# Performance work log

Hardware: AMD Instinct MI355X
Metric: run time of the kernel (lower is better)

Reference implementation:

```python
import jax, jax.numpy as jnp
import numpy as np

DIM = 256
WIN = 8          # window height == width
HEADS = 8
HEAD_DIM = DIM // HEADS
NW = 64          # number of windows per image
B_IMG = 16
N = WIN * WIN    # 64 tokens per window
B_ = B_IMG * NW  # 1024


def _relative_position_index():
    # matches torch.meshgrid default (ij) indexing
    coords = np.stack(np.meshgrid(np.arange(WIN), np.arange(WIN), indexing='ij'))  # [2,Wh,Ww]
    flat = coords.reshape(2, -1)                                # [2,N]
    rel = flat[:, :, None] - flat[:, None, :]                   # [2,N,N]
    rel = rel.transpose(1, 2, 0).copy()                         # [N,N,2]
    rel[:, :, 0] += WIN - 1
    rel[:, :, 1] += WIN - 1
    rel[:, :, 0] *= 2 * WIN - 1
    return rel.sum(-1).astype(np.int32)                         # [N,N]


def setup_inputs() -> dict:
    key = jax.random.key(0)
    ks = jax.random.split(key, 24)
    std = 0.02

    def lin(i):
        W = jax.random.normal(ks[i], (DIM, DIM), jnp.float32) * std
        b = jax.random.normal(ks[i + 1], (DIM,), jnp.float32) * std
        return W, b

    Wq, bq = lin(0)
    Wk, bk = lin(2)
    Wv, bv = lin(4)
    Wvs, bvs = lin(6)      # v_scale
    Wvh, bvh = lin(8)      # v_shift
    Wpx, bpx = lin(10)     # proj_x
    Wps, bps = lin(12)     # proj_scale
    Wph, bph = lin(14)     # proj_shift

    bias_table = jax.random.normal(ks[16], ((2 * WIN - 1) * (2 * WIN - 1), HEADS), jnp.float32) * std
    rel_idx = jnp.asarray(_relative_position_index())

    q_input = jax.random.normal(ks[17], (B_, N, DIM), jnp.float32)
    k_input = jax.random.normal(ks[18], (B_, N, DIM), jnp.float32)
    v_input = jax.random.normal(ks[19], (B_, N, DIM), jnp.float32)
    scale_in = jax.random.normal(ks[20], (B_, N, DIM), jnp.float32)
    shift_in = jax.random.normal(ks[21], (B_, N, DIM), jnp.float32)

    # shifted-window style mask: 0 where attendable, large negative otherwise
    u = jax.random.uniform(ks[22], (NW, N, N), jnp.float32)
    mask = jnp.where(u < 0.15, -100.0, 0.0).astype(jnp.float32)

    return {
        'q_input': q_input, 'k_input': k_input, 'v_input': v_input,
        'scale_in': scale_in, 'shift_in': shift_in, 'mask': mask,
        'Wq': Wq, 'bq': bq, 'Wk': Wk, 'bk': bk, 'Wv': Wv, 'bv': bv,
        'Wvs': Wvs, 'bvs': bvs, 'Wvh': Wvh, 'bvh': bvh,
        'Wpx': Wpx, 'bpx': bpx, 'Wps': Wps, 'bps': bps, 'Wph': Wph, 'bph': bph,
        'bias_table': bias_table, 'rel_idx': rel_idx,
    }


def reference(q_input, k_input, v_input, scale_in, shift_in, mask,
              Wq, bq, Wk, bk, Wv, bv, Wvs, bvs, Wvh, bvh,
              Wpx, bpx, Wps, bps, Wph, bph, bias_table, rel_idx):
    B, Ntok, C = q_input.shape
    scale = HEAD_DIM ** -0.5

    def to_heads(x, W, b):
        # nn.Linear: x @ W.T + b, then split heads -> [B, H, N, hd]
        return (x @ W.T + b).reshape(B, Ntok, HEADS, HEAD_DIM).transpose(0, 2, 1, 3)

    q = to_heads(q_input, Wq, bq) * scale
    k = to_heads(k_input, Wk, bk)
    v = to_heads(v_input, Wv, bv)
    v_scale = to_heads(scale_in, Wvs, bvs)
    v_shift = to_heads(shift_in, Wvh, bvh)

    attn = jnp.einsum('bhnd,bhmd->bhnm', q, k)                    # [B,H,N,N]
    rel_bias = bias_table[rel_idx]                                # [N,N,H] gather
    attn = attn + rel_bias.transpose(2, 0, 1)[None]               # add per-head bias

    nW = mask.shape[0]
    attn = attn.reshape(B // nW, nW, HEADS, Ntok, Ntok) + mask[None, :, None]
    attn = jax.nn.softmax(attn.reshape(B, HEADS, Ntok, Ntok), axis=-1)

    def out_proj(val, Wp, bp):
        o = jnp.einsum('bhnm,bhmd->bhnd', attn, val)
        o = o.transpose(0, 2, 1, 3).reshape(B, Ntok, C)
        return o @ Wp.T + bp

    x_out = out_proj(v, Wpx, bpx)
    scale_out = out_proj(v_scale, Wps, bps)
    shift_out = out_proj(v_shift, Wph, bph)
    return (x_out, scale_out, shift_out)
```

## Files before the change

kernel.cpp:

```cpp
#include <hip/hip_runtime.h>


typedef __attribute__((ext_vector_type(8))) __bf16 bf16x8;
typedef __attribute__((ext_vector_type(4))) float f32x4;
typedef __attribute__((ext_vector_type(4))) unsigned short u16x4;

#define LOFF_QS 16384
#define LOFF_KS 32768
#define LOFF_PS 49152

__device__ __forceinline__ unsigned short f2bf(float f) {
  unsigned int u = __float_as_uint(f);
  u += 0x7FFFu + ((u >> 16) & 1u);
  return (unsigned short)(u >> 16);
}

__device__ __forceinline__ int swz256(int row, int col) {
  return row * 256 + (col ^ ((row & 31) << 3));
}
__device__ __forceinline__ int swz64(int row, int col) {
  return row * 64 + (col ^ ((row & 7) << 3));
}

__global__ void pack_weights(const float* __restrict__ W0, const float* __restrict__ W1,
                             const float* __restrict__ W2, const float* __restrict__ W3,
                             const float* __restrict__ W4, const float* __restrict__ W5,
                             const float* __restrict__ W6, const float* __restrict__ W7,
                             unsigned short* __restrict__ pk) {
  int t = blockIdx.x * 256 + threadIdx.x;
  int wsel = t >> 13;
  int rem  = t & 8191;
  int cb   = rem >> 9;
  int kc   = (rem >> 6) & 7;
  int l    = rem & 63;
  const float* W = (wsel == 0) ? W0 : (wsel == 1) ? W1 : (wsel == 2) ? W2 : (wsel == 3) ? W3
                 : (wsel == 4) ? W4 : (wsel == 5) ? W5 : (wsel == 6) ? W6 : W7;
  int row = cb * 16 + (l & 15);
  int col = kc * 32 + ((l >> 4) << 3);
  const float* src = W + row * 256 + col;
  unsigned short* dst = pk + (size_t)t * 8;
#pragma unroll
  for (int i = 0; i < 8; ++i) dst[i] = f2bf(src[i]);
}

__global__ void make_bm(const float* __restrict__ mask, const float* __restrict__ btab,
                        const int* __restrict__ ridx, float* __restrict__ bm) {
  int t = blockIdx.x * 256 + threadIdx.x;
  int j = t & 63;
  int i = (t >> 6) & 63;
  int h = (t >> 12) & 7;
  int wi = t >> 15;
  bm[t] = mask[(wi * 64 + i) * 64 + j] + btab[ridx[i * 64 + j] * 8 + h];
}

__device__ __forceinline__ void stage_x(unsigned short* XS, const float* __restrict__ X,
                                        int b, int tid) {
  const float4* src = reinterpret_cast<const float4*>(X + (size_t)b * 16384);
#pragma unroll
  for (int it = 0; it < 8; ++it) {
    int f = it * 512 + tid;
    float4 v = src[f];
    int row = f >> 6;
    int col = (f & 63) << 2;
    u16x4 p;
    p[0] = f2bf(v.x); p[1] = f2bf(v.y); p[2] = f2bf(v.z); p[3] = f2bf(v.w);
    *reinterpret_cast<u16x4*>(XS + swz256(row, col)) = p;
  }
}

__device__ __forceinline__ void proj_core(const unsigned short* __restrict__ aTile,
                                          const unsigned short* __restrict__ pw,
                                          const float* __restrict__ bias, float scale,
                                          int lane, int w, f32x4 acc[4][2]) {
  const int r16 = lane & 15, c4 = lane >> 4;
  f32x4 z = {0.f, 0.f, 0.f, 0.f};
#pragma unroll
  for (int mf = 0; mf < 4; ++mf)
#pragma unroll
    for (int nf = 0; nf < 2; ++nf) acc[mf][nf] = z;
#pragma unroll
  for (int kc = 0; kc < 8; ++kc) {
    bf16x8 a[4];
#pragma unroll
    for (int mf = 0; mf < 4; ++mf) {
      int row = mf * 16 + r16;
      int col = kc * 32 + (c4 << 3);
      a[mf] = *reinterpret_cast<const bf16x8*>(aTile + swz256(row, col));
    }
    bf16x8 bb[2];
#pragma unroll
    for (int nf = 0; nf < 2; ++nf)
      bb[nf] = *reinterpret_cast<const bf16x8*>(pw + ((((2 * w + nf) * 8 + kc) * 64 + lane) << 3));
#pragma unroll
    for (int mf = 0; mf < 4; ++mf)
#pragma unroll
      for (int nf = 0; nf < 2; ++nf)
        acc[mf][nf] = __builtin_amdgcn_mfma_f32_16x16x32_bf16(a[mf], bb[nf], acc[mf][nf], 0, 0, 0);
  }
  float b0 = bias[w * 32 + r16];
  float b1 = bias[w * 32 + 16 + r16];
#pragma unroll
  for (int mf = 0; mf < 4; ++mf)
#pragma unroll
    for (int r = 0; r < 4; ++r) {
      acc[mf][0][r] = (acc[mf][0][r] + b0) * scale;
      acc[mf][1][r] = (acc[mf][1][r] + b1) * scale;
    }
}

__device__ __forceinline__ void store_rm_bf16(unsigned short* dst, const f32x4 acc[4][2],
                                              int lane, int w) {
  const int r16 = lane & 15, c4 = lane >> 4;
#pragma unroll
  for (int mf = 0; mf < 4; ++mf)
#pragma unroll
    for (int nf = 0; nf < 2; ++nf)
#pragma unroll
      for (int r = 0; r < 4; ++r) {
        int row = mf * 16 + c4 * 4 + r;
        int col = w * 32 + nf * 16 + r16;
        dst[swz256(row, col)] = f2bf(acc[mf][nf][r]);
      }
}

__device__ __forceinline__ void store_tr_bf16(unsigned short* dst, const f32x4 acc[4][2],
                                              int lane, int w) {
  const int r16 = lane & 15, c4 = lane >> 4;
#pragma unroll
  for (int mf = 0; mf < 4; ++mf)
#pragma unroll
    for (int nf = 0; nf < 2; ++nf)
#pragma unroll
      for (int r = 0; r < 4; ++r) {
        int vrow = w * 32 + nf * 16 + r16;
        int vcol = mf * 16 + c4 * 4 + r;
        dst[swz64(vrow, vcol)] = f2bf(acc[mf][nf][r]);
      }
}

__device__ __forceinline__ void store_gl_f32(float* __restrict__ dst, const f32x4 acc[4][2],
                                             int lane, int w) {
  const int r16 = lane & 15, c4 = lane >> 4;
#pragma unroll
  for (int mf = 0; mf < 4; ++mf)
#pragma unroll
    for (int nf = 0; nf < 2; ++nf)
#pragma unroll
      for (int r = 0; r < 4; ++r) {
        int row = mf * 16 + c4 * 4 + r;
        int col = w * 32 + nf * 16 + r16;
        dst[row * 256 + col] = acc[mf][nf][r];
      }
}

__device__ __forceinline__ void attn_core(const unsigned short* __restrict__ sm,
                                          const float* __restrict__ bmw,
                                          int lane, int w, unsigned short* Ps) {
  const int r16 = lane & 15, c4 = lane >> 4;
  const unsigned short* Qs = sm + LOFF_QS;
  const unsigned short* Ks = sm + LOFF_KS;
  bf16x8 aq[4], bk4[4];
#pragma unroll
  for (int mf = 0; mf < 4; ++mf)
    aq[mf] = *reinterpret_cast<const bf16x8*>(Qs + swz256(mf * 16 + r16, w * 32 + (c4 << 3)));
#pragma unroll
  for (int nf = 0; nf < 4; ++nf)
    bk4[nf] = *reinterpret_cast<const bf16x8*>(Ks + swz256(nf * 16 + r16, w * 32 + (c4 << 3)));
  f32x4 z = {0.f, 0.f, 0.f, 0.f};
  f32x4 s[4][4];
#pragma unroll
  for (int mf = 0; mf < 4; ++mf)
#pragma unroll
    for (int nf = 0; nf < 4; ++nf)
      s[mf][nf] = __builtin_amdgcn_mfma_f32_16x16x32_bf16(aq[mf], bk4[nf], z, 0, 0, 0);
#pragma unroll
  for (int mf = 0; mf < 4; ++mf)
#pragma unroll
    for (int r = 0; r < 4; ++r) {
      int row = mf * 16 + c4 * 4 + r;
      const float* bp = bmw + row * 64 + r16;
      float v0 = s[mf][0][r] + bp[0];
      float v1 = s[mf][1][r] + bp[16];
      float v2 = s[mf][2][r] + bp[32];
      float v3 = s[mf][3][r] + bp[48];
      float m = fmaxf(fmaxf(v0, v1), fmaxf(v2, v3));
      m = fmaxf(m, __shfl_xor(m, 1));
      m = fmaxf(m, __shfl_xor(m, 2));
      m = fmaxf(m, __shfl_xor(m, 4));
      m = fmaxf(m, __shfl_xor(m, 8));
      float e0 = __expf(v0 - m), e1 = __expf(v1 - m);
      float e2 = __expf(v2 - m), e3 = __expf(v3 - m);
      float sum = e0 + e1 + e2 + e3;
      sum += __shfl_xor(sum, 1);
      sum += __shfl_xor(sum, 2);
      sum += __shfl_xor(sum, 4);
      sum += __shfl_xor(sum, 8);
      float inv = 1.0f / sum;
      Ps[swz64(row, r16)]      = f2bf(e0 * inv);
      Ps[swz64(row, r16 + 16)] = f2bf(e1 * inv);
      Ps[swz64(row, r16 + 32)] = f2bf(e2 * inv);
      Ps[swz64(row, r16 + 48)] = f2bf(e3 * inv);
    }
}

__device__ __forceinline__ void pv_core(const unsigned short* __restrict__ Ps,
                                        const unsigned short* __restrict__ Vt,
                                        int lane, int w, f32x4 o[4][2]) {
  const int r16 = lane & 15, c4 = lane >> 4;
  f32x4 z = {0.f, 0.f, 0.f, 0.f};
#pragma unroll
  for (int mf = 0; mf < 4; ++mf)
#pragma unroll
    for (int nf = 0; nf < 2; ++nf) o[mf][nf] = z;
#pragma unroll
  for (int kc = 0; kc < 2; ++kc) {
    bf16x8 a[4];
#pragma unroll
    for (int mf = 0; mf < 4; ++mf)
      a[mf] = *reinterpret_cast<const bf16x8*>(Ps + swz64(mf * 16 + r16, kc * 32 + (c4 << 3)));
    bf16x8 bb[2];
#pragma unroll
    for (int nf = 0; nf < 2; ++nf)
      bb[nf] = *reinterpret_cast<const bf16x8*>(Vt + swz64(w * 32 + nf * 16 + r16, kc * 32 + (c4 << 3)));
#pragma unroll
    for (int mf = 0; mf < 4; ++mf)
#pragma unroll
      for (int nf = 0; nf < 2; ++nf)
        o[mf][nf] = __builtin_amdgcn_mfma_f32_16x16x32_bf16(a[mf], bb[nf], o[mf][nf], 0, 0, 0);
  }
}

__global__ __launch_bounds__(512, 2) void win_attn(
    const float* __restrict__ gq, const float* __restrict__ gk, const float* __restrict__ gv,
    const float* __restrict__ gsc, const float* __restrict__ gsh,
    const unsigned short* __restrict__ pk,
    const float* __restrict__ b_q, const float* __restrict__ b_k, const float* __restrict__ b_v,
    const float* __restrict__ b_vs, const float* __restrict__ b_vh,
    const float* __restrict__ b_px, const float* __restrict__ b_ps, const float* __restrict__ b_ph,
    const float* __restrict__ bm, float* __restrict__ out) {
  __shared__ __align__(16) unsigned short sm[81920];
  const int b    = blockIdx.x;
  const int tid  = threadIdx.x;
  const int lane = tid & 63;
  const int w    = tid >> 6;

  unsigned short* XS = sm;
  unsigned short* QS = sm + LOFF_QS;
  unsigned short* KS = sm + LOFF_KS;
  unsigned short* PS = sm + LOFF_PS + w * 4096;

  f32x4 acc[4][2];

  stage_x(XS, gq, b, tid);
  __syncthreads();
  proj_core(XS, pk, b_q, 0.17677669529663687f, lane, w, acc);
  store_rm_bf16(QS, acc, lane, w);
  __syncthreads();
  stage_x(XS, gk, b, tid);
  __syncthreads();
  proj_core(XS, pk + 65536, b_k, 1.0f, lane, w, acc);
  store_rm_bf16(KS, acc, lane, w);
  __syncthreads();
  stage_x(XS, gv, b, tid);
  attn_core(sm, bm + (size_t)(((b & 63) * 8 + w) << 12), lane, w, PS);
  __syncthreads();
  proj_core(XS, pk + 2 * 65536, b_v, 1.0f, lane, w, acc);
  store_tr_bf16(QS, acc, lane, w);
  __syncthreads();
  stage_x(XS, gsc, b, tid);
  {
    f32x4 o[4][2];
    pv_core(PS, QS, lane, w, o);
    store_rm_bf16(KS, o, lane, w);
  }
  __syncthreads();
  proj_core(KS, pk + 5 * 65536, b_px, 1.0f, lane, w, acc);
  store_gl_f32(out + (size_t)b * 16384, acc, lane, w);
  proj_core(XS, pk + 3 * 65536, b_vs, 1.0f, lane, w, acc);
  store_tr_bf16(QS, acc, lane, w);
  __syncthreads();
  stage_x(XS, gsh, b, tid);
  {
    f32x4 o[4][2];
    pv_core(PS, QS, lane, w, o);
    store_rm_bf16(KS, o, lane, w);
  }
  __syncthreads();
  proj_core(KS, pk + 6 * 65536, b_ps, 1.0f, lane, w, acc);
  store_gl_f32(out + 16777216 + (size_t)b * 16384, acc, lane, w);
  proj_core(XS, pk + 4 * 65536, b_vh, 1.0f, lane, w, acc);
  store_tr_bf16(QS, acc, lane, w);
  __syncthreads();
  {
    f32x4 o[4][2];
    pv_core(PS, QS, lane, w, o);
    store_rm_bf16(KS, o, lane, w);
  }
  __syncthreads();
  proj_core(KS, pk + 7 * 65536, b_ph, 1.0f, lane, w, acc);
  store_gl_f32(out + 33554432 + (size_t)b * 16384, acc, lane, w);
}

extern "C" void kernel_launch(void* const* d_in, const int* in_sizes, int n_in,
                              void* d_out, int out_size, void* d_ws, size_t ws_size,
                              hipStream_t stream) {
  const float* Xq   = (const float*)d_in[0];
  const float* Xk   = (const float*)d_in[1];
  const float* Xv   = (const float*)d_in[2];
  const float* Xsc  = (const float*)d_in[3];
  const float* Xsh  = (const float*)d_in[4];
  const float* mask = (const float*)d_in[5];
  const float* Wq   = (const float*)d_in[6];  const float* bq  = (const float*)d_in[7];
  const float* Wk   = (const float*)d_in[8];  const float* bk  = (const float*)d_in[9];
  const float* Wv   = (const float*)d_in[10]; const float* bv  = (const float*)d_in[11];
  const float* Wvs  = (const float*)d_in[12]; const float* bvs = (const float*)d_in[13];
  const float* Wvh  = (const float*)d_in[14]; const float* bvh = (const float*)d_in[15];
  const float* Wpx  = (const float*)d_in[16]; const float* bpx = (const float*)d_in[17];
  const float* Wps  = (const float*)d_in[18]; const float* bps = (const float*)d_in[19];
  const float* Wph  = (const float*)d_in[20]; const float* bph = (const float*)d_in[21];
  const float* btab = (const float*)d_in[22];
  const int*   ridx = (const int*)d_in[23];

  unsigned short* pk = (unsigned short*)d_ws;
  float* bm = (float*)((char*)d_ws + (size_t)8 * 65536 * 2);

  pack_weights<<<256, 256, 0, stream>>>(Wq, Wk, Wv, Wvs, Wvh, Wpx, Wps, Wph, pk);
  make_bm<<<8192, 256, 0, stream>>>(mask, btab, ridx, bm);
  win_attn<<<1024, 512, 0, stream>>>(Xq, Xk, Xv, Xsc, Xsh, pk,
                                     bq, bk, bv, bvs, bvh, bpx, bps, bph,
                                     bm, (float*)d_out);
}
```

Baseline: 215.3 us.

## Prefetch input tiles into registers to overlap global loads with MFMA compute

Global loads of each input tile are split from the bf16 conversion and LDS write. Loads are issued into register double buffers (rA/rB) one or two stages ahead, so HBM latency is hidden behind projection MFMAs and several barriers disappear. The K tile is staged into the P buffer region before attention runs. The bias+mask table is also re-laid out so each lane reads one float4 instead of four scalars, and bf16 conversion now uses the native cast. This costs 64 extra VGPRs per thread for the two buffers, which may cause spills or lower occupancy under launch_bounds(512,2).

Result: slower. 226.3 us (+5.1%).

```diff
diff --git a/kernel.cpp b/kernel.cpp
--- a/kernel.cpp
+++ b/kernel.cpp
@@ -2,6 +2,7 @@
 
 
 typedef __attribute__((ext_vector_type(8))) __bf16 bf16x8;
+typedef __attribute__((ext_vector_type(4))) __bf16 bf16x4;
 typedef __attribute__((ext_vector_type(4))) float f32x4;
 typedef __attribute__((ext_vector_type(4))) unsigned short u16x4;
 
@@ -10,9 +11,12 @@
 #define LOFF_PS 49152
 
 __device__ __forceinline__ unsigned short f2bf(float f) {
-  unsigned int u = __float_as_uint(f);
-  u += 0x7FFFu + ((u >> 16) & 1u);
-  return (unsigned short)(u >> 16);
+  return __builtin_bit_cast(unsigned short, (__bf16)f);
+}
+__device__ __forceinline__ u16x4 cvt4(float4 v) {
+  bf16x4 h;
+  h[0] = (__bf16)v.x; h[1] = (__bf16)v.y; h[2] = (__bf16)v.z; h[3] = (__bf16)v.w;
+  return __builtin_bit_cast(u16x4, h);
 }
 
 __device__ __forceinline__ int swz256(int row, int col) {
@@ -50,21 +54,24 @@
   int i = (t >> 6) & 63;
   int h = (t >> 12) & 7;
   int wi = t >> 15;
-  bm[t] = mask[(wi * 64 + i) * 64 + j] + btab[ridx[i * 64 + j] * 8 + h];
-}
-
-__device__ __forceinline__ void stage_x(unsigned short* XS, const float* __restrict__ X,
-                                        int b, int tid) {
+  float v = mask[(wi * 64 + i) * 64 + j] + btab[ridx[i * 64 + j] * 8 + h];
+  int idx = (((wi * 8 + h) * 64 + i) * 16 + (j & 15)) * 4 + (j >> 4);
+  bm[idx] = v;
+}
+
+__device__ __forceinline__ void load_tile(float4 r[8], const float* __restrict__ X,
+                                          int b, int tid) {
   const float4* src = reinterpret_cast<const float4*>(X + (size_t)b * 16384);
+#pragma unroll
+  for (int it = 0; it < 8; ++it) r[it] = src[it * 512 + tid];
+}
+__device__ __forceinline__ void write_tile(unsigned short* XS, const float4 r[8], int tid) {
 #pragma unroll
   for (int it = 0; it < 8; ++it) {
     int f = it * 512 + tid;
-    float4 v = src[f];
     int row = f >> 6;
     int col = (f & 63) << 2;
-    u16x4 p;
-    p[0] = f2bf(v.x); p[1] = f2bf(v.y); p[2] = f2bf(v.z); p[3] = f2bf(v.w);
-    *reinterpret_cast<u16x4*>(XS + swz256(row, col)) = p;
+    *reinterpret_cast<u16x4*>(XS + swz256(row, col)) = cvt4(r[it]);
   }
 }
 
@@ -178,11 +185,11 @@
 #pragma unroll
     for (int r = 0; r < 4; ++r) {
       int row = mf * 16 + c4 * 4 + r;
-      const float* bp = bmw + row * 64 + r16;
-      float v0 = s[mf][0][r] + bp[0];
-      float v1 = s[mf][1][r] + bp[16];
-      float v2 = s[mf][2][r] + bp[32];
-      float v3 = s[mf][3][r] + bp[48];
+      float4 bp4 = *reinterpret_cast<const float4*>(bmw + row * 64 + (r16 << 2));
+      float v0 = s[mf][0][r] + bp4.x;
+      float v1 = s[mf][1][r] + bp4.y;
+      float v2 = s[mf][2][r] + bp4.z;
+      float v3 = s[mf][3][r] + bp4.w;
       float m = fmaxf(fmaxf(v0, v1), fmaxf(v2, v3));
       m = fmaxf(m, __shfl_xor(m, 1));
       m = fmaxf(m, __shfl_xor(m, 2));
@@ -247,44 +254,50 @@
   unsigned short* XS = sm;
   unsigned short* QS = sm + LOFF_QS;
   unsigned short* KS = sm + LOFF_KS;
+  unsigned short* PB = sm + LOFF_PS;
   unsigned short* PS = sm + LOFF_PS + w * 4096;
 
   f32x4 acc[4][2];
-
-  stage_x(XS, gq, b, tid);
-  __syncthreads();
+  float4 rA[8], rB[8];
+
+  load_tile(rA, gq, b, tid);
+  load_tile(rB, gk, b, tid);
+  write_tile(XS, rA, tid);
+  __syncthreads();
+  load_tile(rA, gv, b, tid);
   proj_core(XS, pk, b_q, 0.17677669529663687f, lane, w, acc);
   store_rm_bf16(QS, acc, lane, w);
-  __syncthreads();
-  stage_x(XS, gk, b, tid);
-  __syncthreads();
-  proj_core(XS, pk + 65536, b_k, 1.0f, lane, w, acc);
+  write_tile(PB, rB, tid);
+  __syncthreads();
+  load_tile(rB, gsc, b, tid);
+  proj_core(PB, pk + 65536, b_k, 1.0f, lane, w, acc);
   store_rm_bf16(KS, acc, lane, w);
-  __syncthreads();
-  stage_x(XS, gv, b, tid);
+  write_tile(XS, rA, tid);
+  __syncthreads();
   attn_core(sm, bm + (size_t)(((b & 63) * 8 + w) << 12), lane, w, PS);
   __syncthreads();
+  load_tile(rA, gsh, b, tid);
   proj_core(XS, pk + 2 * 65536, b_v, 1.0f, lane, w, acc);
   store_tr_bf16(QS, acc, lane, w);
   __syncthreads();
-  stage_x(XS, gsc, b, tid);
   {
     f32x4 o[4][2];
     pv_core(PS, QS, lane, w, o);
     store_rm_bf16(KS, o, lane, w);
   }
+  write_tile(XS, rB, tid);
   __syncthreads();
   proj_core(KS, pk + 5 * 65536, b_px, 1.0f, lane, w, acc);
   store_gl_f32(out + (size_t)b * 16384, acc, lane, w);
   proj_core(XS, pk + 3 * 65536, b_vs, 1.0f, lane, w, acc);
   store_tr_bf16(QS, acc, lane, w);
   __syncthreads();
-  stage_x(XS, gsh, b, tid);
   {
     f32x4 o[4][2];
     pv_core(PS, QS, lane, w, o);
     store_rm_bf16(KS, o, lane, w);
   }
+  write_tile(XS, rA, tid);
   __syncthreads();
   proj_core(KS, pk + 6 * 65536, b_ps, 1.0f, lane, w, acc);
   store_gl_f32(out + 16777216 + (size_t)b * 16384, acc, lane, w);
```
